# Optimization experiments

Measured on AMD Instinct MI355X. Metric: run time of the kernel, lower is better.

Reference implementation:

```python
import jax, jax.numpy as jnp
import numpy as np

B, N1, N2, C1, C2, MLP_OUT = 16, 4096, 1024, 128, 256, 256


def setup_inputs() -> dict:
    key = jax.random.key(0)
    k = jax.random.split(key, 8)
    xyz1 = jax.random.normal(k[0], (B, N1, 3), dtype=jnp.float32)
    feat1 = jax.random.normal(k[1], (B, N1, C1), dtype=jnp.float32)
    xyz2 = jax.random.normal(k[2], (B, N2, 3), dtype=jnp.float32)
    feat2 = jax.random.normal(k[3], (B, N2, C2), dtype=jnp.float32)
    d_in = C1 + C2
    W1 = jax.random.normal(k[4], (d_in, MLP_OUT), dtype=jnp.float32) / np.sqrt(d_in)
    b1 = jnp.zeros((MLP_OUT,), dtype=jnp.float32)
    W2 = jax.random.normal(k[5], (MLP_OUT, MLP_OUT), dtype=jnp.float32) / np.sqrt(MLP_OUT)
    b2 = jnp.zeros((MLP_OUT,), dtype=jnp.float32)
    return {"xyz1": xyz1, "feat1": feat1, "xyz2": xyz2, "feat2": feat2,
            "W1": W1, "b1": b1, "W2": W2, "b2": b2}


def reference(xyz1, feat1, xyz2, feat2, W1, b1, W2, b2):
    # squared pairwise distances [B, N1, N2]
    dists = jnp.sum((xyz1[:, :, None, :] - xyz2[:, None, :, :]) ** 2, axis=-1)
    # 3 nearest neighbors (smallest distances)
    neg_d3, idx = jax.lax.top_k(-dists, 3)      # [B, N1, 3]
    d3 = jnp.maximum(-neg_d3, 1e-10)
    w = 1.0 / d3
    w = w / jnp.sum(w, axis=-1, keepdims=True)   # [B, N1, 3]
    # gather neighbor features: [B, N1, 3, C2]
    neighbor_feats = jax.vmap(lambda f, i: f[i])(feat2, idx)
    interpolated = jnp.sum(w[..., None] * neighbor_feats, axis=2)  # [B, N1, C2]
    new_feat = jnp.concatenate([interpolated, feat1], axis=-1)     # [B, N1, C2+C1]
    h = jax.nn.relu(new_feat @ W1 + b1)
    return jax.nn.relu(h @ W2 + b2)
```

## Files before the change

kernel.cpp:

```cpp
#include <hip/hip_runtime.h>
#include <cstdint>
#include <cstddef>

typedef unsigned short ushort_t;
typedef unsigned int uint_t;

typedef __bf16 bf16x8 __attribute__((ext_vector_type(8)));
typedef float floatx4 __attribute__((ext_vector_type(4)));

#define B_ 16
#define N1_ 4096
#define N2_ 1024
#define C1_ 128
#define C2_ 256
#define DIN_ 384
#define DOUT_ 256
#define M_ (B_ * N1_)


__device__ __forceinline__ ushort_t f2bf(float f) {
  unsigned int u = __builtin_bit_cast(unsigned int, f);
  u = (u + 0x7fffu + ((u >> 16) & 1u)) >> 16;
  return (ushort_t)u;
}

__device__ __forceinline__ void gload_lds16(const void* g, void* s) {
  __builtin_amdgcn_global_load_lds(
      (__attribute__((address_space(1))) void*)(void*)g,
      (__attribute__((address_space(3))) void*)s, 16, 0, 0);
}


__global__ __launch_bounds__(256) void prep_kernel(
    const float* __restrict__ W1, const float* __restrict__ W2,
    ushort_t* __restrict__ W1t, ushort_t* __restrict__ W2t) {
  int tid = blockIdx.x * 256 + threadIdx.x;
  if (tid < DOUT_ * DIN_) {
    int n = tid / DIN_;
    int k = tid - n * DIN_;
    W1t[tid] = f2bf(W1[(size_t)k * DOUT_ + n]);
  }
  if (tid < DOUT_ * DOUT_) {
    int n = tid >> 8;
    int k = tid & 255;
    W2t[tid] = f2bf(W2[(size_t)k * DOUT_ + n]);
  }
}


__device__ __forceinline__ void ins_exact(float& s0, float& s1, float& s2,
                                          int& i0, int& i1, int& i2,
                                          float d, int p) {
  float ns2 = __builtin_amdgcn_fmed3f(d, s1, s2);
  float ns1 = __builtin_amdgcn_fmed3f(d, s0, s1);
  float ns0 = fminf(d, s0);
  bool c0 = d < s0, c1 = d < s1, c2 = d < s2;
  i2 = c1 ? i1 : (c2 ? p : i2);
  i1 = c0 ? i0 : (c1 ? p : i1);
  i0 = c0 ? p : i0;
  s0 = ns0; s1 = ns1; s2 = ns2;
}

__device__ __forceinline__ void ins_merge(float& s0, float& s1, float& s2,
                                          int& i0, int& i1, int& i2,
                                          float e, int j) {
  bool t0 = (e < s0) || (e == s0 && j < i0);
  bool t1 = (e < s1) || (e == s1 && j < i1);
  bool t2 = (e < s2) || (e == s2 && j < i2);
  s2 = t1 ? s1 : (t2 ? e : s2);
  i2 = t1 ? i1 : (t2 ? j : i2);
  s1 = t0 ? s0 : (t1 ? e : s1);
  i1 = t0 ? i0 : (t1 ? j : i1);
  s0 = t0 ? e : s0;
  i0 = t0 ? j : i0;
}

__global__ __launch_bounds__(256) void knn_kernel(
    const float* __restrict__ xyz1, const float* __restrict__ xyz2,
    int* __restrict__ idx_out, float* __restrict__ w_out) {
  __shared__ float4 xs4[N2_];
  int b = blockIdx.x >> 7;
  int n1base = (blockIdx.x & 127) << 5;
  const float* p2 = xyz2 + (size_t)b * N2_ * 3;
  for (int i = threadIdx.x; i < N2_; i += 256) {
    const float* s = p2 + 3 * i;
    xs4[i] = make_float4(s[0], s[1], s[2], 0.0f);
  }
  __syncthreads();

  int g = threadIdx.x >> 3;
  int sub = threadIdx.x & 7;
  int row = b * N1_ + n1base + g;
  const float* p1 = xyz1 + (size_t)row * 3;
  float x1 = p1[0], y1 = p1[1], z1 = p1[2];

  float s0 = 3.0e38f, s1 = 3.0e38f, s2 = 3.0e38f;
  int i0 = 0, i1 = 0, i2 = 0;

  int p = sub;
#pragma unroll 8
  for (int t = 0; t < N2_ / 8; ++t) {
    float4 q = xs4[p];
    float dx = x1 - q.x;
    float dy = y1 - q.y;
    float dz = z1 - q.z;
    float d = dx * dx + dy * dy + dz * dz;
    ins_exact(s0, s1, s2, i0, i1, i2, d, p);
    p += 8;
  }

#pragma unroll
  for (int m = 1; m <= 4; m <<= 1) {
    float e0 = __shfl_xor(s0, m), e1 = __shfl_xor(s1, m), e2 = __shfl_xor(s2, m);
    int j0 = __shfl_xor(i0, m), j1 = __shfl_xor(i1, m), j2 = __shfl_xor(i2, m);
    ins_merge(s0, s1, s2, i0, i1, i2, e0, j0);
    ins_merge(s0, s1, s2, i0, i1, i2, e1, j1);
    ins_merge(s0, s1, s2, i0, i1, i2, e2, j2);
  }

  if (sub == 0) {
    float r0 = 1.0f / fmaxf(s0, 1e-10f);
    float r1 = 1.0f / fmaxf(s1, 1e-10f);
    float r2 = 1.0f / fmaxf(s2, 1e-10f);
    float s = 1.0f / (r0 + r1 + r2);
    int base = row * 3;
    idx_out[base + 0] = i0;
    idx_out[base + 1] = i1;
    idx_out[base + 2] = i2;
    w_out[base + 0] = r0 * s;
    w_out[base + 1] = r1 * s;
    w_out[base + 2] = r2 * s;
  }
}


__global__ __launch_bounds__(256) void build_kernel(
    const float* __restrict__ feat1, const float* __restrict__ feat2,
    const int* __restrict__ idx, const float* __restrict__ w,
    ushort_t* __restrict__ A1) {
  int wave = threadIdx.x >> 6;
  int lane = threadIdx.x & 63;
  int row = blockIdx.x * 4 + wave;
  int b = row >> 12;

  const int* ip = idx + (size_t)row * 3;
  const float* wp = w + (size_t)row * 3;
  int i0 = ip[0], i1 = ip[1], i2 = ip[2];
  float w0 = wp[0], w1 = wp[1], w2 = wp[2];

  const float4* f0 = (const float4*)(feat2 + ((size_t)b * N2_ + i0) * C2_);
  const float4* f1 = (const float4*)(feat2 + ((size_t)b * N2_ + i1) * C2_);
  const float4* f2 = (const float4*)(feat2 + ((size_t)b * N2_ + i2) * C2_);
  float4 a = f0[lane];
  float4 c = f1[lane];
  float4 d = f2[lane];
  float vx = w0 * a.x + w1 * c.x + w2 * d.x;
  float vy = w0 * a.y + w1 * c.y + w2 * d.y;
  float vz = w0 * a.z + w1 * c.z + w2 * d.z;
  float vw = w0 * a.w + w1 * c.w + w2 * d.w;

  ushort_t* orow = A1 + (size_t)row * DIN_;
  uint_t lo = (uint_t)f2bf(vx) | ((uint_t)f2bf(vy) << 16);
  uint_t hi = (uint_t)f2bf(vz) | ((uint_t)f2bf(vw) << 16);
  ((uint2*)orow)[lane] = make_uint2(lo, hi);

  const float2* g1 = (const float2*)(feat1 + (size_t)row * C1_);
  float2 t = g1[lane];
  uint_t pk = (uint_t)f2bf(t.x) | ((uint_t)f2bf(t.y) << 16);
  *(uint_t*)(orow + C2_ + lane * 2) = pk;
}


template <int K, bool OUT_BF16>
__global__ __launch_bounds__(256, 2) void gemm_kernel(
    const ushort_t* __restrict__ A, const ushort_t* __restrict__ Bt,
    const float* __restrict__ bias, void* __restrict__ out) {
  __shared__ ushort_t As[128 * 32];
  __shared__ ushort_t Bs[256 * 32];
  const int m0 = blockIdx.x * 128;
  const int tid = threadIdx.x;
  const int wave = tid >> 6;
  const int lane = tid & 63;
  const int wm = wave & 1;
  const int wn = wave >> 1;

  floatx4 acc[4][8];
#pragma unroll
  for (int i = 0; i < 4; ++i)
#pragma unroll
    for (int j = 0; j < 8; ++j) acc[i][j] = (floatx4)0.0f;

  const int a_off = (wm * 64 + (lane & 15)) * 32 + (lane >> 4) * 8;
  const int b_off = (wn * 128 + (lane & 15)) * 32 + (lane >> 4) * 8;

  for (int kt = 0; kt < K; kt += 32) {
    __syncthreads();
#pragma unroll
    for (int i = 0; i < 2; ++i) {
      int e = (i * 256 + tid) * 8;
      int r = e >> 5, c = e & 31;
      gload_lds16(A + (size_t)(m0 + r) * K + kt + c, &As[e]);
    }
#pragma unroll
    for (int i = 0; i < 4; ++i) {
      int e = (i * 256 + tid) * 8;
      int r = e >> 5, c = e & 31;
      gload_lds16(Bt + (size_t)r * K + kt + c, &Bs[e]);
    }
    __syncthreads();

    bf16x8 af[4], bfr[8];
#pragma unroll
    for (int i = 0; i < 4; ++i) af[i] = *(const bf16x8*)&As[a_off + i * 512];
#pragma unroll
    for (int j = 0; j < 8; ++j) bfr[j] = *(const bf16x8*)&Bs[b_off + j * 512];
#pragma unroll
    for (int i = 0; i < 4; ++i)
#pragma unroll
      for (int j = 0; j < 8; ++j)
        acc[i][j] =
            __builtin_amdgcn_mfma_f32_16x16x32_bf16(af[i], bfr[j], acc[i][j], 0, 0, 0);
  }

#pragma unroll
  for (int j = 0; j < 8; ++j) {
    int col = wn * 128 + j * 16 + (lane & 15);
    float bv = bias[col];
#pragma unroll
    for (int i = 0; i < 4; ++i) {
      int rbase = m0 + wm * 64 + i * 16 + ((lane >> 4) << 2);
#pragma unroll
      for (int r = 0; r < 4; ++r) {
        float v = acc[i][j][r] + bv;
        v = v > 0.0f ? v : 0.0f;
        size_t off = (size_t)(rbase + r) * DOUT_ + col;
        if constexpr (OUT_BF16)
          ((ushort_t*)out)[off] = f2bf(v);
        else
          ((float*)out)[off] = v;
      }
    }
  }
}


constexpr size_t OFF_W1T = 0;
constexpr size_t OFF_W2T = OFF_W1T + 196608;
constexpr size_t OFF_IDX = OFF_W2T + 131072;
constexpr size_t OFF_W = OFF_IDX + 786432;
constexpr size_t OFF_A1 = OFF_W + 786432;
constexpr size_t OFF_H = OFF_A1 + 50331648;
constexpr size_t WS_TOTAL = OFF_H + 33554432;

extern "C" void kernel_launch(void* const* d_in, const int* in_sizes, int n_in,
                              void* d_out, int out_size, void* d_ws, size_t ws_size,
                              hipStream_t stream) {
  const float* xyz1 = (const float*)d_in[0];
  const float* feat1 = (const float*)d_in[1];
  const float* xyz2 = (const float*)d_in[2];
  const float* feat2 = (const float*)d_in[3];
  const float* W1 = (const float*)d_in[4];
  const float* b1 = (const float*)d_in[5];
  const float* W2 = (const float*)d_in[6];
  const float* b2 = (const float*)d_in[7];

  if (ws_size < WS_TOTAL) return;

  char* ws = (char*)d_ws;
  ushort_t* W1t = (ushort_t*)(ws + OFF_W1T);
  ushort_t* W2t = (ushort_t*)(ws + OFF_W2T);
  int* idx = (int*)(ws + OFF_IDX);
  float* w = (float*)(ws + OFF_W);
  ushort_t* A1 = (ushort_t*)(ws + OFF_A1);
  ushort_t* H = (ushort_t*)(ws + OFF_H);

  prep_kernel<<<384, 256, 0, stream>>>(W1, W2, W1t, W2t);
  knn_kernel<<<B_ * (N1_ / 32), 256, 0, stream>>>(xyz1, xyz2, idx, w);
  build_kernel<<<M_ / 4, 256, 0, stream>>>(feat1, feat2, idx, w, A1);
  gemm_kernel<DIN_, true><<<M_ / 128, 256, 0, stream>>>(A1, W1t, b1, H);
  gemm_kernel<DOUT_, false><<<M_ / 128, 256, 0, stream>>>(H, W2t, b2, (float*)d_out);
}
```

Baseline: 217.4 us.

## Fuse gather-build and both MLP GEMMs into one kernel with LDS-resident activations

Merges the feature gather/interpolation, the first GEMM, and the second GEMM into a single kernel that processes 64 rows per block. The concatenated input row and the hidden activations stay in shared memory (a swizzled layout for H), so the large A1 and H intermediate tensors are never written to or read back from global memory. Weights are pre-tiled into 32-wide k-slabs and read straight from global memory into registers with double buffering. The cost is a smaller M tile, per-block weight re-reads through cache, and 48KB of LDS per block, which may limit occupancy.

Result: faster. 191.6 us (-11.8%).

```diff
diff --git a/kernel.cpp b/kernel.cpp
--- a/kernel.cpp
+++ b/kernel.cpp
@@ -24,26 +24,18 @@
   return (ushort_t)u;
 }
 
-__device__ __forceinline__ void gload_lds16(const void* g, void* s) {
-  __builtin_amdgcn_global_load_lds(
-      (__attribute__((address_space(1))) void*)(void*)g,
-      (__attribute__((address_space(3))) void*)s, 16, 0, 0);
-}
-
 
 __global__ __launch_bounds__(256) void prep_kernel(
     const float* __restrict__ W1, const float* __restrict__ W2,
-    ushort_t* __restrict__ W1t, ushort_t* __restrict__ W2t) {
-  int tid = blockIdx.x * 256 + threadIdx.x;
-  if (tid < DOUT_ * DIN_) {
-    int n = tid / DIN_;
-    int k = tid - n * DIN_;
-    W1t[tid] = f2bf(W1[(size_t)k * DOUT_ + n]);
-  }
-  if (tid < DOUT_ * DOUT_) {
-    int n = tid >> 8;
-    int k = tid & 255;
-    W2t[tid] = f2bf(W2[(size_t)k * DOUT_ + n]);
+    ushort_t* __restrict__ W1s, ushort_t* __restrict__ W2s) {
+  int e = blockIdx.x * 256 + threadIdx.x;
+  if (e < DOUT_ * DIN_) {
+    int kk = e & 31, n = (e >> 5) & 255, t = e >> 13;
+    W1s[e] = f2bf(W1[(size_t)(t * 32 + kk) * DOUT_ + n]);
+  }
+  if (e < DOUT_ * DOUT_) {
+    int kk = e & 31, n = (e >> 5) & 255, t = e >> 13;
+    W2s[e] = f2bf(W2[(size_t)(t * 32 + kk) * DOUT_ + n]);
   }
 }
 
@@ -100,19 +92,19 @@
   int p = sub;
 #pragma unroll 8
   for (int t = 0; t < N2_ / 8; ++t) {
-    float4 q = xs4[p];
-    float dx = x1 - q.x;
-    float dy = y1 - q.y;
-    float dz = z1 - q.z;
+    float4 qv = xs4[p];
+    float dx = x1 - qv.x;
+    float dy = y1 - qv.y;
+    float dz = z1 - qv.z;
     float d = dx * dx + dy * dy + dz * dz;
     ins_exact(s0, s1, s2, i0, i1, i2, d, p);
     p += 8;
   }
 
 #pragma unroll
-  for (int m = 1; m <= 4; m <<= 1) {
-    float e0 = __shfl_xor(s0, m), e1 = __shfl_xor(s1, m), e2 = __shfl_xor(s2, m);
-    int j0 = __shfl_xor(i0, m), j1 = __shfl_xor(i1, m), j2 = __shfl_xor(i2, m);
+  for (int mm = 1; mm <= 4; mm <<= 1) {
+    float e0 = __shfl_xor(s0, mm), e1 = __shfl_xor(s1, mm), e2 = __shfl_xor(s2, mm);
+    int j0 = __shfl_xor(i0, mm), j1 = __shfl_xor(i1, mm), j2 = __shfl_xor(i2, mm);
     ins_merge(s0, s1, s2, i0, i1, i2, e0, j0);
     ins_merge(s0, s1, s2, i0, i1, i2, e1, j1);
     ins_merge(s0, s1, s2, i0, i1, i2, e2, j2);
@@ -134,123 +126,188 @@
 }
 
 
-__global__ __launch_bounds__(256) void build_kernel(
+__global__ __launch_bounds__(256, 2) void fused_kernel(
     const float* __restrict__ feat1, const float* __restrict__ feat2,
     const int* __restrict__ idx, const float* __restrict__ w,
-    ushort_t* __restrict__ A1) {
-  int wave = threadIdx.x >> 6;
-  int lane = threadIdx.x & 63;
-  int row = blockIdx.x * 4 + wave;
-  int b = row >> 12;
-
-  const int* ip = idx + (size_t)row * 3;
-  const float* wp = w + (size_t)row * 3;
-  int i0 = ip[0], i1 = ip[1], i2 = ip[2];
-  float w0 = wp[0], w1 = wp[1], w2 = wp[2];
-
-  const float4* f0 = (const float4*)(feat2 + ((size_t)b * N2_ + i0) * C2_);
-  const float4* f1 = (const float4*)(feat2 + ((size_t)b * N2_ + i1) * C2_);
-  const float4* f2 = (const float4*)(feat2 + ((size_t)b * N2_ + i2) * C2_);
-  float4 a = f0[lane];
-  float4 c = f1[lane];
-  float4 d = f2[lane];
-  float vx = w0 * a.x + w1 * c.x + w2 * d.x;
-  float vy = w0 * a.y + w1 * c.y + w2 * d.y;
-  float vz = w0 * a.z + w1 * c.z + w2 * d.z;
-  float vw = w0 * a.w + w1 * c.w + w2 * d.w;
-
-  ushort_t* orow = A1 + (size_t)row * DIN_;
-  uint_t lo = (uint_t)f2bf(vx) | ((uint_t)f2bf(vy) << 16);
-  uint_t hi = (uint_t)f2bf(vz) | ((uint_t)f2bf(vw) << 16);
-  ((uint2*)orow)[lane] = make_uint2(lo, hi);
-
-  const float2* g1 = (const float2*)(feat1 + (size_t)row * C1_);
-  float2 t = g1[lane];
-  uint_t pk = (uint_t)f2bf(t.x) | ((uint_t)f2bf(t.y) << 16);
-  *(uint_t*)(orow + C2_ + lane * 2) = pk;
-}
-
-
-template <int K, bool OUT_BF16>
-__global__ __launch_bounds__(256, 2) void gemm_kernel(
-    const ushort_t* __restrict__ A, const ushort_t* __restrict__ Bt,
-    const float* __restrict__ bias, void* __restrict__ out) {
-  __shared__ ushort_t As[128 * 32];
-  __shared__ ushort_t Bs[256 * 32];
-  const int m0 = blockIdx.x * 128;
+    const ushort_t* __restrict__ W1s, const float* __restrict__ b1,
+    const ushort_t* __restrict__ W2s, const float* __restrict__ b2,
+    float* __restrict__ out) {
+  __shared__ ushort_t As[64 * 384];
   const int tid = threadIdx.x;
   const int wave = tid >> 6;
   const int lane = tid & 63;
-  const int wm = wave & 1;
-  const int wn = wave >> 1;
-
-  floatx4 acc[4][8];
+  const int m = lane & 15;
+  const int q = lane >> 4;
+  const int row0 = blockIdx.x * 64;
+  const int b = row0 >> 12;
+
+#pragma unroll 4
+  for (int it = 0; it < 16; ++it) {
+    int rl = wave * 16 + it;
+    int row = row0 + rl;
+    const int* ip = idx + (size_t)row * 3;
+    const float* wp = w + (size_t)row * 3;
+    int i0 = ip[0], i1 = ip[1], i2 = ip[2];
+    float w0 = wp[0], w1 = wp[1], w2 = wp[2];
+
+    const float4* f0 = (const float4*)(feat2 + ((size_t)b * N2_ + i0) * C2_);
+    const float4* f1 = (const float4*)(feat2 + ((size_t)b * N2_ + i1) * C2_);
+    const float4* f2 = (const float4*)(feat2 + ((size_t)b * N2_ + i2) * C2_);
+    float4 a = f0[lane];
+    float4 c = f1[lane];
+    float4 d = f2[lane];
+    float vx = w0 * a.x + w1 * c.x + w2 * d.x;
+    float vy = w0 * a.y + w1 * c.y + w2 * d.y;
+    float vz = w0 * a.z + w1 * c.z + w2 * d.z;
+    float vw = w0 * a.w + w1 * c.w + w2 * d.w;
+    uint_t lo = (uint_t)f2bf(vx) | ((uint_t)f2bf(vy) << 16);
+    uint_t hi = (uint_t)f2bf(vz) | ((uint_t)f2bf(vw) << 16);
+    int e = (lane >> 3) * 2048 + rl * 32 + ((4 * lane) & 31);
+    *(uint2*)&As[e] = make_uint2(lo, hi);
+
+    float2 t1 = ((const float2*)(feat1 + (size_t)row * C1_))[lane];
+    uint_t pk = (uint_t)f2bf(t1.x) | ((uint_t)f2bf(t1.y) << 16);
+    int e1 = (8 + (lane >> 4)) * 2048 + rl * 32 + ((2 * lane) & 31);
+    *(uint_t*)&As[e1] = pk;
+  }
+  __syncthreads();
+
+  const int b_off = (wave * 64 + m) * 32 + q * 8;
+  const int a_base = m * 32 + q * 8;
+
+  floatx4 acc[4][4];
 #pragma unroll
   for (int i = 0; i < 4; ++i)
 #pragma unroll
-    for (int j = 0; j < 8; ++j) acc[i][j] = (floatx4)0.0f;
-
-  const int a_off = (wm * 64 + (lane & 15)) * 32 + (lane >> 4) * 8;
-  const int b_off = (wn * 128 + (lane & 15)) * 32 + (lane >> 4) * 8;
-
-  for (int kt = 0; kt < K; kt += 32) {
-    __syncthreads();
-#pragma unroll
-    for (int i = 0; i < 2; ++i) {
-      int e = (i * 256 + tid) * 8;
-      int r = e >> 5, c = e & 31;
-      gload_lds16(A + (size_t)(m0 + r) * K + kt + c, &As[e]);
+    for (int j = 0; j < 4; ++j) acc[i][j] = (floatx4)0.0f;
+
+  {
+    bf16x8 bf0[4], bf1[4], af[4];
+#pragma unroll
+    for (int j = 0; j < 4; ++j)
+      bf0[j] = *(const bf16x8*)(W1s + b_off + j * 512);
+#pragma unroll
+    for (int t = 0; t < 12; t += 2) {
+#pragma unroll
+      for (int j = 0; j < 4; ++j)
+        bf1[j] = *(const bf16x8*)(W1s + (size_t)(t + 1) * 8192 + b_off + j * 512);
+#pragma unroll
+      for (int i = 0; i < 4; ++i)
+        af[i] = *(const bf16x8*)&As[t * 2048 + a_base + i * 512];
+#pragma unroll
+      for (int i = 0; i < 4; ++i)
+#pragma unroll
+        for (int j = 0; j < 4; ++j)
+          acc[i][j] = __builtin_amdgcn_mfma_f32_16x16x32_bf16(af[i], bf0[j],
+                                                              acc[i][j], 0, 0, 0);
+      if (t + 2 < 12) {
+#pragma unroll
+        for (int j = 0; j < 4; ++j)
+          bf0[j] = *(const bf16x8*)(W1s + (size_t)(t + 2) * 8192 + b_off + j * 512);
+      }
+#pragma unroll
+      for (int i = 0; i < 4; ++i)
+        af[i] = *(const bf16x8*)&As[(t + 1) * 2048 + a_base + i * 512];
+#pragma unroll
+      for (int i = 0; i < 4; ++i)
+#pragma unroll
+        for (int j = 0; j < 4; ++j)
+          acc[i][j] = __builtin_amdgcn_mfma_f32_16x16x32_bf16(af[i], bf1[j],
+                                                              acc[i][j], 0, 0, 0);
     }
-#pragma unroll
-    for (int i = 0; i < 4; ++i) {
-      int e = (i * 256 + tid) * 8;
-      int r = e >> 5, c = e & 31;
-      gload_lds16(Bt + (size_t)r * K + kt + c, &Bs[e]);
-    }
-    __syncthreads();
-
-    bf16x8 af[4], bfr[8];
-#pragma unroll
-    for (int i = 0; i < 4; ++i) af[i] = *(const bf16x8*)&As[a_off + i * 512];
-#pragma unroll
-    for (int j = 0; j < 8; ++j) bfr[j] = *(const bf16x8*)&Bs[b_off + j * 512];
+  }
+  __syncthreads();
+
+  ushort_t* HS = As;
+#pragma unroll
+  for (int j = 0; j < 4; ++j) {
+    int col = wave * 64 + j * 16 + m;
+    float bv = b1[col];
+    int cb = (col >> 3) & 3;
+    int tb = (col >> 5) * 2048 + (col & 7);
 #pragma unroll
     for (int i = 0; i < 4; ++i)
 #pragma unroll
-      for (int j = 0; j < 8; ++j)
-        acc[i][j] =
-            __builtin_amdgcn_mfma_f32_16x16x32_bf16(af[i], bfr[j], acc[i][j], 0, 0, 0);
-  }
-
-#pragma unroll
-  for (int j = 0; j < 8; ++j) {
-    int col = wn * 128 + j * 16 + (lane & 15);
-    float bv = bias[col];
-#pragma unroll
-    for (int i = 0; i < 4; ++i) {
-      int rbase = m0 + wm * 64 + i * 16 + ((lane >> 4) << 2);
-#pragma unroll
       for (int r = 0; r < 4; ++r) {
+        int row = i * 16 + q * 4 + r;
         float v = acc[i][j][r] + bv;
         v = v > 0.0f ? v : 0.0f;
-        size_t off = (size_t)(rbase + r) * DOUT_ + col;
-        if constexpr (OUT_BF16)
-          ((ushort_t*)out)[off] = f2bf(v);
-        else
-          ((float*)out)[off] = v;
-      }
+        int ch = cb ^ ((row >> 2) & 3);
+        HS[tb + row * 32 + ch * 8] = f2bf(v);
+      }
+  }
+  __syncthreads();
+
+  floatx4 acc2[4][4];
+#pragma unroll
+  for (int i = 0; i < 4; ++i)
+#pragma unroll
+    for (int j = 0; j < 4; ++j) acc2[i][j] = (floatx4)0.0f;
+
+  {
+    bf16x8 bf0[4], bf1[4], af[4];
+#pragma unroll
+    for (int j = 0; j < 4; ++j)
+      bf0[j] = *(const bf16x8*)(W2s + b_off + j * 512);
+#pragma unroll
+    for (int t = 0; t < 8; t += 2) {
+#pragma unroll
+      for (int j = 0; j < 4; ++j)
+        bf1[j] = *(const bf16x8*)(W2s + (size_t)(t + 1) * 8192 + b_off + j * 512);
+#pragma unroll
+      for (int i = 0; i < 4; ++i) {
+        int row = m + 16 * i;
+        int ch = q ^ ((row >> 2) & 3);
+        af[i] = *(const bf16x8*)&HS[t * 2048 + row * 32 + ch * 8];
+      }
+#pragma unroll
+      for (int i = 0; i < 4; ++i)
+#pragma unroll
+        for (int j = 0; j < 4; ++j)
+          acc2[i][j] = __builtin_amdgcn_mfma_f32_16x16x32_bf16(af[i], bf0[j],
+                                                               acc2[i][j], 0, 0, 0);
+      if (t + 2 < 8) {
+#pragma unroll
+        for (int j = 0; j < 4; ++j)
+          bf0[j] = *(const bf16x8*)(W2s + (size_t)(t + 2) * 8192 + b_off + j * 512);
+      }
+#pragma unroll
+      for (int i = 0; i < 4; ++i) {
+        int row = m + 16 * i;
+        int ch = q ^ ((row >> 2) & 3);
+        af[i] = *(const bf16x8*)&HS[(t + 1) * 2048 + row * 32 + ch * 8];
+      }
+#pragma unroll
+      for (int i = 0; i < 4; ++i)
+#pragma unroll
+        for (int j = 0; j < 4; ++j)
+          acc2[i][j] = __builtin_amdgcn_mfma_f32_16x16x32_bf16(af[i], bf1[j],
+                                                               acc2[i][j], 0, 0, 0);
     }
   }
-}
-
-
-constexpr size_t OFF_W1T = 0;
-constexpr size_t OFF_W2T = OFF_W1T + 196608;
-constexpr size_t OFF_IDX = OFF_W2T + 131072;
+
+#pragma unroll
+  for (int j = 0; j < 4; ++j) {
+    int col = wave * 64 + j * 16 + m;
+    float bv = b2[col];
+#pragma unroll
+    for (int i = 0; i < 4; ++i)
+#pragma unroll
+      for (int r = 0; r < 4; ++r) {
+        int row = i * 16 + q * 4 + r;
+        float v = acc2[i][j][r] + bv;
+        v = v > 0.0f ? v : 0.0f;
+        out[(size_t)(row0 + row) * DOUT_ + col] = v;
+      }
+  }
+}
+
+
+constexpr size_t OFF_W1S = 0;
+constexpr size_t OFF_W2S = OFF_W1S + 196608;
+constexpr size_t OFF_IDX = OFF_W2S + 131072;
 constexpr size_t OFF_W = OFF_IDX + 786432;
-constexpr size_t OFF_A1 = OFF_W + 786432;
-constexpr size_t OFF_H = OFF_A1 + 50331648;
-constexpr size_t WS_TOTAL = OFF_H + 33554432;
+constexpr size_t WS_TOTAL = OFF_W + 786432;
 
 extern "C" void kernel_launch(void* const* d_in, const int* in_sizes, int n_in,
                               void* d_out, int out_size, void* d_ws, size_t ws_size,
@@ -267,16 +324,13 @@
   if (ws_size < WS_TOTAL) return;
 
   char* ws = (char*)d_ws;
-  ushort_t* W1t = (ushort_t*)(ws + OFF_W1T);
-  ushort_t* W2t = (ushort_t*)(ws + OFF_W2T);
+  ushort_t* W1s = (ushort_t*)(ws + OFF_W1S);
+  ushort_t* W2s = (ushort_t*)(ws + OFF_W2S);
   int* idx = (int*)(ws + OFF_IDX);
   float* w = (float*)(ws + OFF_W);
-  ushort_t* A1 = (ushort_t*)(ws + OFF_A1);
-  ushort_t* H = (ushort_t*)(ws + OFF_H);
-
-  prep_kernel<<<384, 256, 0, stream>>>(W1, W2, W1t, W2t);
+
+  prep_kernel<<<384, 256, 0, stream>>>(W1, W2, W1s, W2s);
   knn_kernel<<<B_ * (N1_ / 32), 256, 0, stream>>>(xyz1, xyz2, idx, w);
-  build_kernel<<<M_ / 4, 256, 0, stream>>>(feat1, feat2, idx, w, A1);
-  gemm_kernel<DIN_, true><<<M_ / 128, 256, 0, stream>>>(A1, W1t, b1, H);
-  gemm_kernel<DOUT_, false><<<M_ / 128, 256, 0, stream>>>(H, W2t, b2, (float*)d_out);
-}
+  fused_kernel<<<M_ / 64, 256, 0, stream>>>(feat1, feat2, idx, w, W1s, b1, W2s,
+                                            b2, (float*)d_out);
+}
```
